# Performance work log

Measured on AMD Instinct MI355X. Metric: run time of the kernel, lower is better.

## Reference

```python
import jax, jax.numpy as jnp
import numpy as np

NUM_Q = 4096  # C.NUM_OF_QUESTIONS
MAX_STEP = 200  # C.MAX_STEP
B = 64
EPS = 1e-8


def setup_inputs() -> dict:
    key = jax.random.key(0)
    k1, k2 = jax.random.split(key)
    # pred: probabilities in (0,1), shape [B, MAX_STEP-1, NUM_Q]
    pred = jax.random.uniform(k1, (B, MAX_STEP - 1, NUM_Q), dtype=jnp.float32)
    # batch: binary response encoding, shape [B, MAX_STEP, 2*NUM_Q]
    batch = jax.random.bernoulli(k2, 0.5, (B, MAX_STEP, 2 * NUM_Q)).astype(jnp.float32)
    return {"pred": pred, "batch": batch}


def reference(pred, batch):
    # Targets at t+1 aligned with predictions at t.
    tgt = batch[:, 1:MAX_STEP, :]            # [B, T-1, 2*NUM_Q]
    mask_q = tgt[..., :NUM_Q]                # answered correctly -> -log(p)
    mask_nq = tgt[..., NUM_Q:]               # answered incorrectly -> -log(1-p)
    loss = -jnp.sum(mask_q * jnp.log(pred + EPS) + mask_nq * jnp.log(1.0 - pred + EPS))
    return loss
```

## Files before the change

### kernel.cpp

```cpp
#include <hip/hip_runtime.h>

#define NUM_Q 4096
#define MAX_STEP 200
#define NBATCH 64
#define NT 199
#define EPS 1e-8f
#define NQ4 (NUM_Q / 4)
#define TOTAL_V4 (NBATCH * NT * NQ4)
#define NBLK 1024

__global__ __launch_bounds__(256) void loss_main(const float* __restrict__ pred,
                                                 const float* __restrict__ batch,
                                                 float* __restrict__ blockSums) {
    const float4* __restrict__ pred4 = (const float4*)pred;
    const int stride = NBLK * 256;

    float acc = 0.0f;
    for (int g = blockIdx.x * 256 + threadIdx.x; g < TOTAL_V4; g += stride) {
        const int row = g >> 10;
        const int r   = g & (NQ4 - 1);
        const int b   = row / NT;
        const int t   = row - b * NT;
        const float4* __restrict__ bq =
            (const float4*)(batch + ((size_t)(b * MAX_STEP + t + 1) << 13));

        float4 p  = pred4[g];
        float4 mq = bq[r];
        float4 mn = bq[r + NQ4];
        acc += mq.x * __logf(p.x + EPS) + mn.x * __logf(1.0f - p.x + EPS);
        acc += mq.y * __logf(p.y + EPS) + mn.y * __logf(1.0f - p.y + EPS);
        acc += mq.z * __logf(p.z + EPS) + mn.z * __logf(1.0f - p.z + EPS);
        acc += mq.w * __logf(p.w + EPS) + mn.w * __logf(1.0f - p.w + EPS);
    }

    #pragma unroll
    for (int off = 32; off > 0; off >>= 1)
        acc += __shfl_down(acc, off, 64);

    __shared__ float smem[4];
    const int lane = threadIdx.x & 63;
    const int wave = threadIdx.x >> 6;
    if (lane == 0) smem[wave] = acc;
    __syncthreads();
    if (threadIdx.x == 0)
        blockSums[blockIdx.x] = smem[0] + smem[1] + smem[2] + smem[3];
}

__global__ __launch_bounds__(256) void loss_final(const float* __restrict__ blockSums,
                                                  float* __restrict__ out) {
    float acc = 0.0f;
    #pragma unroll
    for (int k = 0; k < NBLK / 256; ++k)
        acc += blockSums[threadIdx.x + k * 256];

    #pragma unroll
    for (int off = 32; off > 0; off >>= 1)
        acc += __shfl_down(acc, off, 64);

    __shared__ float smem[4];
    const int lane = threadIdx.x & 63;
    const int wave = threadIdx.x >> 6;
    if (lane == 0) smem[wave] = acc;
    __syncthreads();
    if (threadIdx.x == 0)
        out[0] = -(smem[0] + smem[1] + smem[2] + smem[3]);
}

extern "C" void kernel_launch(void* const* d_in, const int* in_sizes, int n_in,
                              void* d_out, int out_size, void* d_ws, size_t ws_size,
                              hipStream_t stream) {
    const float* pred  = (const float*)d_in[0];
    const float* batch = (const float*)d_in[1];
    float* blockSums   = (float*)d_ws;
    float* out         = (float*)d_out;

    loss_main<<<NBLK, 256, 0, stream>>>(pred, batch, blockSums);
    loss_final<<<1, 256, 0, stream>>>(blockSums, out);
}
```

Measured before the change: 640.9 us.

## Map one block per row and issue all row loads upfront

Replaces the grid-stride loop over 1024 blocks with one block per (batch, step) row. Each thread loads four float4 chunks of pred and of both mask halves before computing. The per-element row/batch index math goes away, and many more loads are in flight at once to hide memory latency. The cost is a larger grid and a final reduction over 12736 partial sums instead of 1024.

```diff
diff --git a/kernel.cpp b/kernel.cpp
--- a/kernel.cpp
+++ b/kernel.cpp
@@ -4,34 +4,46 @@
 #define MAX_STEP 200
 #define NBATCH 64
 #define NT 199
+#define NROWS (NBATCH * NT)
 #define EPS 1e-8f
 #define NQ4 (NUM_Q / 4)
-#define TOTAL_V4 (NBATCH * NT * NQ4)
-#define NBLK 1024
 
 __global__ __launch_bounds__(256) void loss_main(const float* __restrict__ pred,
                                                  const float* __restrict__ batch,
                                                  float* __restrict__ blockSums) {
-    const float4* __restrict__ pred4 = (const float4*)pred;
-    const int stride = NBLK * 256;
+    const int row = blockIdx.x;
+    const int b = row / NT;
+    const int t = row - b * NT;
+
+    const float4* __restrict__ predRow = (const float4*)(pred + (size_t)row * NUM_Q);
+    const float*  batchRow = batch + ((size_t)(b * MAX_STEP + t + 1) << 13);
+    const float4* __restrict__ mqRow  = (const float4*)(batchRow);
+    const float4* __restrict__ mnqRow = (const float4*)(batchRow + NUM_Q);
+
+    float4 p0  = predRow[threadIdx.x];
+    float4 p1  = predRow[threadIdx.x + 256];
+    float4 p2  = predRow[threadIdx.x + 512];
+    float4 p3  = predRow[threadIdx.x + 768];
+    float4 q0  = mqRow[threadIdx.x];
+    float4 q1  = mqRow[threadIdx.x + 256];
+    float4 q2  = mqRow[threadIdx.x + 512];
+    float4 q3  = mqRow[threadIdx.x + 768];
+    float4 n0  = mnqRow[threadIdx.x];
+    float4 n1  = mnqRow[threadIdx.x + 256];
+    float4 n2  = mnqRow[threadIdx.x + 512];
+    float4 n3  = mnqRow[threadIdx.x + 768];
 
     float acc = 0.0f;
-    for (int g = blockIdx.x * 256 + threadIdx.x; g < TOTAL_V4; g += stride) {
-        const int row = g >> 10;
-        const int r   = g & (NQ4 - 1);
-        const int b   = row / NT;
-        const int t   = row - b * NT;
-        const float4* __restrict__ bq =
-            (const float4*)(batch + ((size_t)(b * MAX_STEP + t + 1) << 13));
-
-        float4 p  = pred4[g];
-        float4 mq = bq[r];
-        float4 mn = bq[r + NQ4];
-        acc += mq.x * __logf(p.x + EPS) + mn.x * __logf(1.0f - p.x + EPS);
-        acc += mq.y * __logf(p.y + EPS) + mn.y * __logf(1.0f - p.y + EPS);
-        acc += mq.z * __logf(p.z + EPS) + mn.z * __logf(1.0f - p.z + EPS);
-        acc += mq.w * __logf(p.w + EPS) + mn.w * __logf(1.0f - p.w + EPS);
-    }
+    #define TERM(q, n, p) \
+        acc += q.x * __logf(p.x + EPS) + n.x * __logf(1.0f - p.x + EPS); \
+        acc += q.y * __logf(p.y + EPS) + n.y * __logf(1.0f - p.y + EPS); \
+        acc += q.z * __logf(p.z + EPS) + n.z * __logf(1.0f - p.z + EPS); \
+        acc += q.w * __logf(p.w + EPS) + n.w * __logf(1.0f - p.w + EPS);
+    TERM(q0, n0, p0)
+    TERM(q1, n1, p1)
+    TERM(q2, n2, p2)
+    TERM(q3, n3, p3)
+    #undef TERM
 
     #pragma unroll
     for (int off = 32; off > 0; off >>= 1)
@@ -43,15 +55,14 @@
     if (lane == 0) smem[wave] = acc;
     __syncthreads();
     if (threadIdx.x == 0)
-        blockSums[blockIdx.x] = smem[0] + smem[1] + smem[2] + smem[3];
+        blockSums[row] = smem[0] + smem[1] + smem[2] + smem[3];
 }
 
 __global__ __launch_bounds__(256) void loss_final(const float* __restrict__ blockSums,
                                                   float* __restrict__ out) {
     float acc = 0.0f;
-    #pragma unroll
-    for (int k = 0; k < NBLK / 256; ++k)
-        acc += blockSums[threadIdx.x + k * 256];
+    for (int i = threadIdx.x; i < NROWS; i += 256)
+        acc += blockSums[i];
 
     #pragma unroll
     for (int off = 32; off > 0; off >>= 1)
@@ -74,6 +85,6 @@
     float* blockSums   = (float*)d_ws;
     float* out         = (float*)d_out;
 
-    loss_main<<<NBLK, 256, 0, stream>>>(pred, batch, blockSums);
+    loss_main<<<NROWS, 256, 0, stream>>>(pred, batch, blockSums);
     loss_final<<<1, 256, 0, stream>>>(blockSums, out);
 }
```

Result: slower. 655.1 us (+2.2%).

## Increase grid size, software-prefetch next iteration, and use nontemporal loads

Applied to the files above, without the earlier changes.

Raises the block count so each thread handles a fixed eight iterations, and fully unrolls the loop with next-iteration loads issued before the current log computations. Loads use nontemporal hints to avoid polluting caches with streamed data. The final reduction becomes a strided loop to handle the larger block count. This aims to expose more memory-level parallelism in a bandwidth-bound streaming reduction, at the cost of more registers and a larger partial-sum array.

```diff
diff --git a/kernel.cpp b/kernel.cpp
--- a/kernel.cpp
+++ b/kernel.cpp
@@ -4,33 +4,54 @@
 #define MAX_STEP 200
 #define NBATCH 64
 #define NT 199
+#define NROWS (NBATCH * NT)
 #define EPS 1e-8f
 #define NQ4 (NUM_Q / 4)
-#define TOTAL_V4 (NBATCH * NT * NQ4)
-#define NBLK 1024
+#define TOTAL_V4 (NROWS * NQ4)
+#define NBLK 6368
+#define ITERS (TOTAL_V4 / (NBLK * 256))
+
+typedef float vf4 __attribute__((ext_vector_type(4)));
 
 __global__ __launch_bounds__(256) void loss_main(const float* __restrict__ pred,
                                                  const float* __restrict__ batch,
                                                  float* __restrict__ blockSums) {
-    const float4* __restrict__ pred4 = (const float4*)pred;
+    const vf4* __restrict__ pred4 = (const vf4*)pred;
     const int stride = NBLK * 256;
+    int g = blockIdx.x * 256 + threadIdx.x;
 
     float acc = 0.0f;
-    for (int g = blockIdx.x * 256 + threadIdx.x; g < TOTAL_V4; g += stride) {
-        const int row = g >> 10;
-        const int r   = g & (NQ4 - 1);
-        const int b   = row / NT;
-        const int t   = row - b * NT;
-        const float4* __restrict__ bq =
-            (const float4*)(batch + ((size_t)(b * MAX_STEP + t + 1) << 13));
 
-        float4 p  = pred4[g];
-        float4 mq = bq[r];
-        float4 mn = bq[r + NQ4];
-        acc += mq.x * __logf(p.x + EPS) + mn.x * __logf(1.0f - p.x + EPS);
-        acc += mq.y * __logf(p.y + EPS) + mn.y * __logf(1.0f - p.y + EPS);
-        acc += mq.z * __logf(p.z + EPS) + mn.z * __logf(1.0f - p.z + EPS);
-        acc += mq.w * __logf(p.w + EPS) + mn.w * __logf(1.0f - p.w + EPS);
+    vf4 p, q, n;
+    {
+        const int row = g >> 10, r = g & (NQ4 - 1);
+        const int b = row / NT, t = row - b * NT;
+        const vf4* __restrict__ bq =
+            (const vf4*)(batch + ((size_t)(b * MAX_STEP + t + 1) << 13));
+        p = __builtin_nontemporal_load(&pred4[g]);
+        q = __builtin_nontemporal_load(&bq[r]);
+        n = __builtin_nontemporal_load(&bq[r + NQ4]);
+    }
+
+    #pragma unroll
+    for (int i = 0; i < ITERS; ++i) {
+        vf4 p2 = {0,0,0,0}, q2 = {0,0,0,0}, n2 = {0,0,0,0};
+        const int gn = g + stride;
+        if (i + 1 < ITERS) {
+            const int row = gn >> 10, r = gn & (NQ4 - 1);
+            const int b = row / NT, t = row - b * NT;
+            const vf4* __restrict__ bq =
+                (const vf4*)(batch + ((size_t)(b * MAX_STEP + t + 1) << 13));
+            p2 = __builtin_nontemporal_load(&pred4[gn]);
+            q2 = __builtin_nontemporal_load(&bq[r]);
+            n2 = __builtin_nontemporal_load(&bq[r + NQ4]);
+        }
+        acc += q.x * __logf(p.x + EPS) + n.x * __logf(1.0f - p.x + EPS);
+        acc += q.y * __logf(p.y + EPS) + n.y * __logf(1.0f - p.y + EPS);
+        acc += q.z * __logf(p.z + EPS) + n.z * __logf(1.0f - p.z + EPS);
+        acc += q.w * __logf(p.w + EPS) + n.w * __logf(1.0f - p.w + EPS);
+        p = p2; q = q2; n = n2;
+        g = gn;
     }
 
     #pragma unroll
@@ -49,9 +70,8 @@
 __global__ __launch_bounds__(256) void loss_final(const float* __restrict__ blockSums,
                                                   float* __restrict__ out) {
     float acc = 0.0f;
-    #pragma unroll
-    for (int k = 0; k < NBLK / 256; ++k)
-        acc += blockSums[threadIdx.x + k * 256];
+    for (int i = threadIdx.x; i < NBLK; i += 256)
+        acc += blockSums[i];
 
     #pragma unroll
     for (int off = 32; off > 0; off >>= 1)
```

Measured after the change: 617.6 us, median of 2. 3.6% less time.
